# Performance work log

Hardware: AMD Instinct MI355X
Metric: run time of the kernel (lower is better)

Reference implementation:

```python
import jax, jax.numpy as jnp
import numpy as np

B, T, E, H, N = 256, 8, 768, 768, 20000


def setup_inputs() -> dict:
    key = jax.random.key(0)
    ks = jax.random.split(key, 10)
    s = lambda k, shape, sc=1.0: jax.random.normal(k, shape, dtype=jnp.float32) * sc
    return {
        "current_sample_encodings": s(ks[0], (B, E)),
        "example_encodings": s(ks[1], (B, T, E)),
        "all_example_encodings": s(ks[2], (N, E)),
        "policy_example_indices": jax.random.randint(ks[3], (B, T), 0, N, dtype=jnp.int32),
        "W_init": s(ks[4], (E, H), E ** -0.5),
        "b_init": jnp.zeros((H,), jnp.float32),
        "Wx": s(ks[5], (E, 3 * H), E ** -0.5),
        "Wh": s(ks[6], (H, 3 * H), H ** -0.5),
        "bx": jnp.zeros((3 * H,), jnp.float32),
        "bh": jnp.zeros((3 * H,), jnp.float32),
        "bilinear": s(ks[7], (H, E), H ** -0.5),
        "vfe_w": s(ks[8], (H,), H ** -0.5),
        "vfe_b": jnp.zeros((), jnp.float32),
    }


def reference(current_sample_encodings, example_encodings, all_example_encodings,
              policy_example_indices, W_init, b_init, Wx, Wh, bx, bh,
              bilinear, vfe_w, vfe_b):
    Bb, Tt, Ee = example_encodings.shape

    # --- get_latent_states: GRU over example encodings, h0 from current sample ---
    h0 = jnp.tanh(current_sample_encodings @ W_init + b_init)  # [B,H]

    def gru_step(h, x):
        gx = x @ Wx + bx                      # [B,3H]
        gh = h @ Wh + bh                      # [B,3H]
        xr, xz, xn = jnp.split(gx, 3, axis=-1)
        hr, hz, hn = jnp.split(gh, 3, axis=-1)
        r = jax.nn.sigmoid(xr + hr)
        z = jax.nn.sigmoid(xz + hz)
        n = jnp.tanh(xn + r * hn)
        h_new = (1.0 - z) * n + z * h
        return h_new, h_new

    xs = jnp.swapaxes(example_encodings[:, :-1], 0, 1)   # [T-1,B,E]
    _, hs = jax.lax.scan(gru_step, h0, xs)               # [T-1,B,H]
    latent = jnp.concatenate([h0[None], hs], axis=0)     # [T,B,H]

    # --- bilinear query vectors and scoring against the full corpus ---
    query = jnp.einsum('tbh,he->tbe', latent, bilinear)          # [T,B,E]
    acts = jnp.einsum('tbe,ne->tbn', query, all_example_encodings)  # [T,B,N]

    # --- fused scatter masking: -inf at indices of previously chosen examples ---
    neg_inf = jnp.float32(-jnp.inf)

    def mask_step(used, inp):
        a_t, idx_t = inp                                  # [B,N], [B]
        out = jnp.where(used, neg_inf, a_t)
        used = used.at[jnp.arange(Bb), idx_t].set(True)
        return used, out

    used0 = jnp.zeros((Bb, acts.shape[-1]), dtype=bool)
    idxs = jnp.swapaxes(policy_example_indices, 0, 1)     # [T,B]
    _, masked = jax.lax.scan(mask_step, used0, (acts, idxs))  # [T,B,N]

    activations = jnp.swapaxes(masked, 0, 1).reshape(Bb * Tt, -1)  # [B*T,N]

    latent_bt = jnp.swapaxes(latent, 0, 1)                # [B,T,H]
    value_estimates = (latent_bt @ vfe_w + vfe_b).reshape(-1)  # [B*T]
    return activations, value_estimates
```

## Files before the change

### kernel.cpp

```cpp
#include <hip/hip_runtime.h>
#include <math.h>
#include <float.h>

constexpr int Bb = 256, Tt = 8, Ee = 768, Hh = 768, Nn = 20000;
constexpr int H3 = 3 * Hh;

__device__ inline float mask_val() { return __uint_as_float(0xFF7F0000u); }

typedef __attribute__((ext_vector_type(8))) short bf16x8;
typedef __attribute__((ext_vector_type(4))) float f32x4;

__device__ inline unsigned short bf16rne(float x) {
    unsigned u = __float_as_uint(x);
    return (unsigned short)((u + 0x7FFFu + ((u >> 16) & 1)) >> 16);
}
__device__ inline unsigned pk2(float a, float b) {
    return (unsigned)bf16rne(a) | ((unsigned)bf16rne(b) << 16);
}
__device__ inline float sigm(float x) { return 1.f / (1.f + expf(-x)); }

__device__ inline void glds16(const void* g, void* l) {
    __builtin_amdgcn_global_load_lds(
        (const __attribute__((address_space(1))) void*)g,
        (__attribute__((address_space(3))) void*)l, 16, 0, 0);
}

__global__ __launch_bounds__(256) void cvt_all(const float* __restrict__ a, unsigned* __restrict__ oa, int na8,
                                               const float* __restrict__ b, unsigned* __restrict__ ob, int nb8,
                                               const float* __restrict__ c, unsigned* __restrict__ oc, int nc8)
{
    int i = blockIdx.x * 256 + threadIdx.x;
    const float* src; unsigned* dst;
    if (i < na8)            { src = a; dst = oa; }
    else if (i < na8 + nb8) { i -= na8; src = b; dst = ob; }
    else                    { i -= na8 + nb8; if (i >= nc8) return; src = c; dst = oc; }
    const float4* p = (const float4*)(src + (size_t)i * 8);
    float4 x = p[0], y = p[1];
    uint4 v;
    v.x = pk2(x.x, x.y); v.y = pk2(x.z, x.w);
    v.z = pk2(y.x, y.y); v.w = pk2(y.z, y.w);
    *(uint4*)(dst + (size_t)i * 4) = v;
}

__global__ __launch_bounds__(256) void trans_cvt(const float* __restrict__ in, int R, int C,
                                                 unsigned short* __restrict__ out)
{
    __shared__ float tile[32][33];
    int c0 = blockIdx.x * 32, r0 = blockIdx.y * 32;
    int t = threadIdx.x;
    int row = t >> 3, c4 = (t & 7) * 4;
    float4 v = *(const float4*)(in + (size_t)(r0 + row) * C + c0 + c4);
    tile[row][c4+0] = v.x; tile[row][c4+1] = v.y;
    tile[row][c4+2] = v.z; tile[row][c4+3] = v.w;
    __syncthreads();
    int crow = t >> 3, r4 = (t & 7) * 4;
    ushort4 o;
    o.x = bf16rne(tile[r4+0][crow]);
    o.y = bf16rne(tile[r4+1][crow]);
    o.z = bf16rne(tile[r4+2][crow]);
    o.w = bf16rne(tile[r4+3][crow]);
    *(ushort4*)(out + (size_t)(c0 + crow) * R + r0 + r4) = o;
}

__global__ __launch_bounds__(256) void trans_wh(const float* __restrict__ in,
                                                unsigned short* __restrict__ out)
{
    __shared__ float tile[32][33];
    int c0 = blockIdx.x * 32, r0 = blockIdx.y * 32;
    int t = threadIdx.x;
    int row = t >> 3, c4 = (t & 7) * 4;
    float4 v = *(const float4*)(in + (size_t)(r0 + row) * H3 + c0 + c4);
    tile[row][c4+0] = v.x; tile[row][c4+1] = v.y;
    tile[row][c4+2] = v.z; tile[row][c4+3] = v.w;
    __syncthreads();
    int crow = t >> 3, r4 = (t & 7) * 4;
    int cc = c0 + crow;
    int g = cc / Hh, ch = cc - g * Hh;
    int rho = (ch >> 6) * 192 + g * 64 + (ch & 63);
    ushort4 o;
    o.x = bf16rne(tile[r4+0][crow]);
    o.y = bf16rne(tile[r4+1][crow]);
    o.z = bf16rne(tile[r4+2][crow]);
    o.w = bf16rne(tile[r4+3][crow]);
    *(ushort4*)(out + (size_t)rho * Hh + r0 + r4) = o;
}

__global__ __launch_bounds__(256) void gemm_big64(const unsigned short* __restrict__ A,
                                                  const unsigned short* __restrict__ B,
                                                  float* __restrict__ C)
{
    constexpr int BUF = 32768;
    __shared__ char lds[2 * BUF];
    const int t = threadIdx.x;
    const int l = t & 63, w = t >> 6;
    const int wm = (w >> 1) * 64, wn = (w & 1) * 64;

    int id = (blockIdx.x & 7) * 314 + (blockIdx.x >> 3);
    const int bm = (id & 15) * 128;
    const int bn = (id >> 4) * 128;

    const int srow = t >> 3, sslot = t & 7;
    const char* gA[4]; const char* gB[4];
    #pragma unroll
    for (int p = 0; p < 4; ++p) {
        int rp = p * 32 + srow;
        int oct = sslot ^ ((rp >> 1) & 7);
        gA[p] = (const char*)A + (size_t)(bm + rp) * (Ee * 2) + oct * 16;
        int gn = bn + rp; if (gn > Nn - 1) gn = Nn - 1;
        gB[p] = (const char*)B + (size_t)gn * (Ee * 2) + oct * 16;
    }
    const int dbase = t * 16;

    int rAo[4][2], rBo[4][2];
    #pragma unroll
    for (int i = 0; i < 4; ++i) {
        int Ra = wm + i * 16 + (l & 15);
        int Rb = wn + i * 16 + (l & 15);
        #pragma unroll
        for (int ko = 0; ko < 2; ++ko) {
            rAo[i][ko] = Ra * 128 + ((((l >> 4) + 4 * ko) ^ ((Ra >> 1) & 7)) * 16);
            rBo[i][ko] = 16384 + Rb * 128 + ((((l >> 4) + 4 * ko) ^ ((Rb >> 1) & 7)) * 16);
        }
    }

    f32x4 acc[4][4];
    #pragma unroll
    for (int i = 0; i < 4; ++i)
        #pragma unroll
        for (int j = 0; j < 4; ++j)
            acc[i][j] = (f32x4){0.f, 0.f, 0.f, 0.f};

    #pragma unroll
    for (int p = 0; p < 4; ++p) {
        glds16(gA[p], lds + p * 4096 + dbase);
        glds16(gB[p], lds + 16384 + p * 4096 + dbase);
    }
    __syncthreads();

    int cur = 0;
    for (int kt = 0; kt < 12; ++kt) {
        if (kt + 1 < 12) {
            int kb = (kt + 1) * 128;
            char* nb = lds + (cur ^ 1) * BUF;
            #pragma unroll
            for (int p = 0; p < 4; ++p) {
                glds16(gA[p] + kb, nb + p * 4096 + dbase);
                glds16(gB[p] + kb, nb + 16384 + p * 4096 + dbase);
            }
        }
        const char* base = lds + cur * BUF;
        bf16x8 af[4][2], bf[4][2];
        #pragma unroll
        for (int i = 0; i < 4; ++i)
            #pragma unroll
            for (int ko = 0; ko < 2; ++ko) {
                af[i][ko] = *(const bf16x8*)(base + rAo[i][ko]);
                bf[i][ko] = *(const bf16x8*)(base + rBo[i][ko]);
            }
        #pragma unroll
        for (int ko = 0; ko < 2; ++ko)
            #pragma unroll
            for (int i = 0; i < 4; ++i)
                #pragma unroll
                for (int j = 0; j < 4; ++j)
                    acc[i][j] = __builtin_amdgcn_mfma_f32_16x16x32_bf16(af[i][ko], bf[j][ko], acc[i][j], 0, 0, 0);
        __syncthreads();
        cur ^= 1;
    }

    #pragma unroll
    for (int i = 0; i < 4; ++i) {
        int gm = bm + wm + i * 16 + (l >> 4) * 4;
        #pragma unroll
        for (int j = 0; j < 4; ++j) {
            int gn = bn + wn + j * 16 + (l & 15);
            if (gn < Nn) {
                #pragma unroll
                for (int q = 0; q < 4; ++q)
                    C[(size_t)(gm + q) * Nn + gn] = acc[i][j][q];
            }
        }
    }
}

template<int TM, bool CLAMP, bool BIAS, int ACT, int OMODE>
__global__ __launch_bounds__(256) void gemm_mfma(const unsigned short* __restrict__ A, int lda,
                                                 const unsigned short* __restrict__ B,
                                                 const float* __restrict__ bias,
                                                 float* __restrict__ C, int ldc,
                                                 unsigned short* __restrict__ Cbf,
                                                 int M, int N, int K, int nsec)
{
    constexpr int AG  = (TM >= 64) ? TM / 64 : 1;
    constexpr int AB  = TM * 64;
    constexpr int BUF = (TM + 128) * 64;
    constexpr int FM  = (TM >= 64) ? 4 : 2;
    constexpr int FN  = (TM == 128) ? 4 : 2;
    __shared__ char lds[2 * BUF];
    const int t = threadIdx.x;

    int by, bx;
    {
        int id = ((blockIdx.x & 7) * (gridDim.x >> 3)) + (blockIdx.x >> 3);
        by = id / nsec; bx = id - by * nsec;
    }
    const int bm = by * TM, bn = bx * 128;

    const int l = t & 63, w = t >> 6;
    const int wm = (TM == 128) ? (w >> 1) * 64 : 0;
    const int wn = (TM == 128) ? (w & 1) * 64 : w * 32;

    const int sr = w * 16 + (l >> 2);
    const int slot = l & 3;

    const char* gA[AG]; int lA[AG];
    #pragma unroll
    for (int p = 0; p < AG; ++p) {
        int r = p * 64 + sr;
        int rr = (TM == 32) ? (r & 31) : r;
        int oct = slot ^ ((rr >> 1) & 3);
        gA[p] = (const char*)A + (size_t)(bm + rr) * lda * 2 + oct * 16;
        lA[p] = p * 4096 + w * 1024;
    }
    const char* gB[2]; int lB[2];
    #pragma unroll
    for (int p = 0; p < 2; ++p) {
        int r = p * 64 + sr;
        int oct = slot ^ ((r >> 1) & 3);
        int gn = bn + r;
        if (CLAMP) gn = (gn > N - 1) ? (N - 1) : gn;
        gB[p] = (const char*)B + (size_t)gn * K * 2 + oct * 16;
        lB[p] = AB + p * 4096 + w * 1024;
    }

    int rAo[FM], rBo[FN];
    #pragma unroll
    for (int i = 0; i < FM; ++i) {
        int Ra = wm + i * 16 + (l & 15);
        rAo[i] = Ra * 64 + (((l >> 4) ^ ((Ra >> 1) & 3)) * 16);
    }
    #pragma unroll
    for (int j = 0; j < FN; ++j) {
        int Rb = wn + j * 16 + (l & 15);
        rBo[j] = AB + Rb * 64 + (((l >> 4) ^ ((Rb >> 1) & 3)) * 16);
    }

    f32x4 acc[FM][FN];
    #pragma unroll
    for (int i = 0; i < FM; ++i)
        #pragma unroll
        for (int j = 0; j < FN; ++j)
            acc[i][j] = (f32x4){0.f, 0.f, 0.f, 0.f};

    if (TM > 32 || w < 2) {
        #pragma unroll
        for (int p = 0; p < AG; ++p) glds16(gA[p], lds + lA[p]);
    }
    #pragma unroll
    for (int p = 0; p < 2;  ++p) glds16(gB[p], lds + lB[p]);
    __syncthreads();

    int cur = 0;
    for (int k0 = 0; k0 < K; k0 += 32) {
        if (k0 + 32 < K) {
            int kb = (k0 + 32) * 2;
            char* nb = lds + (cur ^ 1) * BUF;
            if (TM > 32 || w < 2) {
                #pragma unroll
                for (int p = 0; p < AG; ++p) glds16(gA[p] + kb, nb + lA[p]);
            }
            #pragma unroll
            for (int p = 0; p < 2;  ++p) glds16(gB[p] + kb, nb + lB[p]);
        }
        const char* base = lds + cur * BUF;
        bf16x8 af[FM], bf[FN];
        #pragma unroll
        for (int i = 0; i < FM; ++i) af[i] = *(const bf16x8*)(base + rAo[i]);
        #pragma unroll
        for (int j = 0; j < FN; ++j) bf[j] = *(const bf16x8*)(base + rBo[j]);
        #pragma unroll
        for (int i = 0; i < FM; ++i)
            #pragma unroll
            for (int j = 0; j < FN; ++j)
                acc[i][j] = __builtin_amdgcn_mfma_f32_16x16x32_bf16(af[i], bf[j], acc[i][j], 0, 0, 0);
        __syncthreads();
        cur ^= 1;
    }

    #pragma unroll
    for (int i = 0; i < FM; ++i) {
        int gm = bm + wm + i * 16 + (l >> 4) * 4;
        #pragma unroll
        for (int j = 0; j < FN; ++j) {
            int gn = bn + wn + j * 16 + (l & 15);
            if (!CLAMP || gn < N) {
                #pragma unroll
                for (int q = 0; q < 4; ++q) {
                    float v = acc[i][j][q];
                    if (BIAS) v += bias[gn];
                    if (ACT == 1) v = tanhf(v);
                    if (OMODE & 1) C[(size_t)(gm + q) * ldc + gn] = v;
                    if (OMODE & 2) Cbf[(size_t)(gm + q) * ldc + gn] = bf16rne(v);
                }
            }
        }
    }
}

__global__ __launch_bounds__(256) void gru_fused(const unsigned short* __restrict__ latbf_t,
                                                 const unsigned short* __restrict__ WhG,
                                                 const float* __restrict__ gx_t,
                                                 const float* __restrict__ bh,
                                                 const float* __restrict__ latent_t,
                                                 float* __restrict__ latent_t1,
                                                 unsigned short* __restrict__ latbf_t1)
{
    constexpr int LDA = Tt * Hh;
    constexpr int LDG = Tt * H3;
    constexpr int ABY = 4096;
    constexpr int BUF = ABY + 24576;
    __shared__ char lds[2 * BUF];
    const int t = threadIdx.x;
    const int mb = blockIdx.x & 7, cb = blockIdx.x >> 3;
    const int bm = mb * 32;

    const int l = t & 63, w = t >> 6;
    const int srow = t >> 3;
    const int sslot = t & 7;

    const char* gA = (const char*)latbf_t + (size_t)(bm + srow) * (LDA * 2)
                   + ((sslot ^ ((srow >> 1) & 7)) * 16);
    const int dA = w * 1024;

    const char* gB[6]; int dB[6];
    #pragma unroll
    for (int p = 0; p < 6; ++p) {
        int rp = p * 32 + srow;
        gB[p] = (const char*)WhG + (size_t)(cb * 192 + rp) * (Hh * 2)
              + ((sslot ^ ((rp >> 1) & 7)) * 16);
        dB[p] = ABY + p * 4096 + w * 1024;
    }

    int rAo[2][2], rBo[3][2];
    #pragma unroll
    for (int i = 0; i < 2; ++i) {
        int Ra = i * 16 + (l & 15);
        #pragma unroll
        for (int ko = 0; ko < 2; ++ko)
            rAo[i][ko] = Ra * 128 + ((((l >> 4) + 4 * ko) ^ ((Ra >> 1) & 7)) * 16);
    }
    #pragma unroll
    for (int g = 0; g < 3; ++g) {
        int Rb = g * 64 + w * 16 + (l & 15);
        #pragma unroll
        for (int ko = 0; ko < 2; ++ko)
            rBo[g][ko] = ABY + Rb * 128 + ((((l >> 4) + 4 * ko) ^ ((Rb >> 1) & 7)) * 16);
    }

    f32x4 acc[2][3];
    #pragma unroll
    for (int i = 0; i < 2; ++i)
        #pragma unroll
        for (int g = 0; g < 3; ++g)
            acc[i][g] = (f32x4){0.f, 0.f, 0.f, 0.f};

    glds16(gA, lds + dA);
    #pragma unroll
    for (int p = 0; p < 6; ++p) glds16(gB[p], lds + dB[p]);
    __syncthreads();

    int cur = 0;
    for (int kt = 0; kt < 12; ++kt) {
        if (kt + 1 < 12) {
            int kb = (kt + 1) * 128;
            char* nb = lds + (cur ^ 1) * BUF;
            glds16(gA + kb, nb + dA);
            #pragma unroll
            for (int p = 0; p < 6; ++p) glds16(gB[p] + kb, nb + dB[p]);
        }
        const char* base = lds + cur * BUF;
        bf16x8 af[2][2], bfr[3][2];
        #pragma unroll
        for (int i = 0; i < 2; ++i)
            #pragma unroll
            for (int ko = 0; ko < 2; ++ko) af[i][ko] = *(const bf16x8*)(base + rAo[i][ko]);
        #pragma unroll
        for (int g = 0; g < 3; ++g)
            #pragma unroll
            for (int ko = 0; ko < 2; ++ko) bfr[g][ko] = *(const bf16x8*)(base + rBo[g][ko]);
        #pragma unroll
        for (int ko = 0; ko < 2; ++ko)
            #pragma unroll
            for (int i = 0; i < 2; ++i)
                #pragma unroll
                for (int g = 0; g < 3; ++g)
                    acc[i][g] = __builtin_amdgcn_mfma_f32_16x16x32_bf16(af[i][ko], bfr[g][ko], acc[i][g], 0, 0, 0);
        __syncthreads();
        cur ^= 1;
    }

    const int colj = cb * 64 + w * 16 + (l & 15);
    const float bhr = bh[colj], bhz = bh[Hh + colj], bhn = bh[2 * Hh + colj];
    #pragma unroll
    for (int i = 0; i < 2; ++i) {
        int row0 = bm + i * 16 + (l >> 4) * 4;
        #pragma unroll
        for (int q = 0; q < 4; ++q) {
            int b = row0 + q;
            const float* gxr = gx_t + (size_t)b * LDG;
            float xr = gxr[colj], xz = gxr[Hh + colj], xn = gxr[2 * Hh + colj];
            float r = sigm(xr + acc[i][0][q] + bhr);
            float z = sigm(xz + acc[i][1][q] + bhz);
            float n = tanhf(xn + r * (acc[i][2][q] + bhn));
            float hprev = latent_t[(size_t)b * LDA + colj];
            float hnew = (1.f - z) * n + z * hprev;
            latent_t1[(size_t)b * LDA + colj] = hnew;
            latbf_t1[(size_t)b * LDA + colj] = bf16rne(hnew);
        }
    }
}

__global__ void mask_kernel(const int* __restrict__ idx, float* __restrict__ out)
{
    int b = threadIdx.x;
    if (b >= Bb) return;
    float mv = mask_val();
    for (int ts = 0; ts < Tt - 1; ++ts) {
        int id = idx[b * Tt + ts];
        for (int t = ts + 1; t < Tt; ++t)
            out[(size_t)(b * Tt + t) * Nn + id] = mv;
    }
}

__global__ void value_kernel(const float* __restrict__ latent,
                             const float* __restrict__ w,
                             const float* __restrict__ b0,
                             float* __restrict__ out)
{
    int row = blockIdx.x;
    int lane = threadIdx.x;
    const float* lr = latent + (size_t)row * Hh;
    float s = 0.f;
    for (int j = lane; j < Hh; j += 64) s += lr[j] * w[j];
    #pragma unroll
    for (int m = 32; m; m >>= 1) s += __shfl_xor(s, m, 64);
    if (lane == 0) out[row] = s + b0[0];
}

extern "C" void kernel_launch(void* const* d_in, const int* in_sizes, int n_in,
                              void* d_out, int out_size, void* d_ws, size_t ws_size,
                              hipStream_t stream)
{
    const float* cur  = (const float*)d_in[0];
    const float* ex   = (const float*)d_in[1];
    const float* alle = (const float*)d_in[2];
    const int*   pidx = (const int*)  d_in[3];
    const float* Wi   = (const float*)d_in[4];
    const float* bi   = (const float*)d_in[5];
    const float* Wx   = (const float*)d_in[6];
    const float* Wh   = (const float*)d_in[7];
    const float* bx   = (const float*)d_in[8];
    const float* bh   = (const float*)d_in[9];
    const float* bil  = (const float*)d_in[10];
    const float* vw   = (const float*)d_in[11];
    const float* vb   = (const float*)d_in[12];
    float* out = (float*)d_out;

    float* ws     = (float*)d_ws;
    float* latent = ws;
    float* gx_all = latent + (size_t)Bb*Tt*Hh;
    float* ghb    = gx_all + (size_t)Bb*Tt*H3;
    float* query  = ghb    + (size_t)Bb*H3;
    unsigned short* alle_bf  = (unsigned short*)(query + (size_t)Bb*Tt*Ee);
    unsigned short* query_bf = alle_bf  + (size_t)Nn*Ee;
    unsigned short* ex_bf    = query_bf + (size_t)Bb*Tt*Ee;
    unsigned short* cur_bf   = ex_bf    + (size_t)Bb*Tt*Ee;
    unsigned short* lat_bf   = cur_bf   + (size_t)Bb*Ee;
    unsigned short* WiT_bf   = lat_bf   + (size_t)Bb*Tt*Hh;
    unsigned short* WxT_bf   = WiT_bf   + (size_t)Hh*Ee;
    unsigned short* WhG_bf   = WxT_bf   + (size_t)H3*Ee;
    unsigned short* bilT_bf  = WhG_bf   + (size_t)H3*Hh;

    dim3 blk(256);

    {
        int na8 = Nn*Ee/8, nb8 = Bb*Tt*Ee/8, nc8 = Bb*Ee/8;
        cvt_all<<<dim3((na8+nb8+nc8+255)/256), blk, 0, stream>>>(
            alle, (unsigned*)alle_bf, na8, ex, (unsigned*)ex_bf, nb8,
            cur, (unsigned*)cur_bf, nc8);
    }
    trans_cvt<<<dim3(Hh/32, Ee/32), blk, 0, stream>>>(Wi,  Ee, Hh, WiT_bf);
    trans_cvt<<<dim3(H3/32, Ee/32), blk, 0, stream>>>(Wx,  Ee, H3, WxT_bf);
    trans_wh <<<dim3(H3/32, Hh/32), blk, 0, stream>>>(Wh,  WhG_bf);
    trans_cvt<<<dim3(Ee/32, Hh/32), blk, 0, stream>>>(bil, Hh, Ee, bilT_bf);

    gemm_mfma<32,false,true,1,3><<<dim3((Bb/32)*(Hh/128)), blk, 0, stream>>>(
        cur_bf, Ee, WiT_bf, bi, latent, Tt*Hh, lat_bf, Bb, Hh, Ee, Hh/128);

    gemm_mfma<128,false,true,0,1><<<dim3((Bb*Tt/128)*(H3/128)), blk, 0, stream>>>(
        ex_bf, Ee, WxT_bf, bx, gx_all, H3, nullptr, Bb*Tt, H3, Ee, H3/128);

    for (int t = 0; t < Tt - 1; ++t) {
        gru_fused<<<dim3(96), blk, 0, stream>>>(
            lat_bf + (size_t)t*Hh, WhG_bf, gx_all + (size_t)t*H3, bh,
            latent + (size_t)t*Hh, latent + (size_t)(t+1)*Hh, lat_bf + (size_t)(t+1)*Hh);
    }

    gemm_mfma<128,false,false,0,2><<<dim3((Bb*Tt/128)*(Ee/128)), blk, 0, stream>>>(
        lat_bf, Hh, bilT_bf, nullptr, query, Ee, query_bf, Bb*Tt, Ee, Hh, Ee/128);

    gemm_big64<<<dim3(157*16), blk, 0, stream>>>(query_bf, alle_bf, out);

    mask_kernel<<<dim3(1), blk, 0, stream>>>(pidx, out);
    value_kernel<<<dim3(Bb*Tt), dim3(64), 0, stream>>>(latent, vw, vb,
                                                       out + (size_t)Bb*Tt*Nn);
}
```

Before: 253.0 us.

## Triple-buffer big scoring GEMM with K=32 stages and single barrier per step

Replaces the double-buffered 128-wide K-tile pipeline of the large corpus-scoring GEMM with a three-stage ring of 64-wide K tiles. It prefetches two tiles ahead, waits on vmcnt explicitly and uses one barrier per iteration instead of two syncs. The goal is to overlap global-to-LDS loads with MFMA work better and to halve the LDS footprint, which may allow more blocks per CU. The cost is twice as many iterations and barriers, and it relies on the vmcnt counting being right for correctness.

```diff
diff --git a/kernel.cpp b/kernel.cpp
--- a/kernel.cpp
+++ b/kernel.cpp
@@ -24,6 +24,8 @@
         (const __attribute__((address_space(1))) void*)g,
         (__attribute__((address_space(3))) void*)l, 16, 0, 0);
 }
+
+#define SCHED __builtin_amdgcn_sched_barrier(0)
 
 __global__ __launch_bounds__(256) void cvt_all(const float* __restrict__ a, unsigned* __restrict__ oa, int na8,
                                                const float* __restrict__ b, unsigned* __restrict__ ob, int nb8,
@@ -85,12 +87,13 @@
     *(ushort4*)(out + (size_t)rho * Hh + r0 + r4) = o;
 }
 
-__global__ __launch_bounds__(256) void gemm_big64(const unsigned short* __restrict__ A,
-                                                  const unsigned short* __restrict__ B,
-                                                  float* __restrict__ C)
-{
-    constexpr int BUF = 32768;
-    __shared__ char lds[2 * BUF];
+__global__ __launch_bounds__(256) void gemm_bigp(const unsigned short* __restrict__ A,
+                                                 const unsigned short* __restrict__ B,
+                                                 float* __restrict__ C)
+{
+    constexpr int NT  = 24;
+    constexpr int BUF = 16384;
+    __shared__ char lds[3 * BUF];
     const int t = threadIdx.x;
     const int l = t & 63, w = t >> 6;
     const int wm = (w >> 1) * 64, wn = (w & 1) * 64;
@@ -99,28 +102,28 @@
     const int bm = (id & 15) * 128;
     const int bn = (id >> 4) * 128;
 
-    const int srow = t >> 3, sslot = t & 7;
-    const char* gA[4]; const char* gB[4];
-    #pragma unroll
-    for (int p = 0; p < 4; ++p) {
-        int rp = p * 32 + srow;
-        int oct = sslot ^ ((rp >> 1) & 7);
-        gA[p] = (const char*)A + (size_t)(bm + rp) * (Ee * 2) + oct * 16;
-        int gn = bn + rp; if (gn > Nn - 1) gn = Nn - 1;
+    const int sr = w * 16 + (l >> 2);
+    const int slot = l & 3;
+    const char* gA[2]; const char* gB[2];
+    int dA[2], dB[2];
+    #pragma unroll
+    for (int p = 0; p < 2; ++p) {
+        int r = p * 64 + sr;
+        int oct = slot ^ ((r >> 1) & 3);
+        gA[p] = (const char*)A + (size_t)(bm + r) * (Ee * 2) + oct * 16;
+        dA[p] = p * 4096 + w * 1024;
+        int gn = bn + r; if (gn > Nn - 1) gn = Nn - 1;
         gB[p] = (const char*)B + (size_t)gn * (Ee * 2) + oct * 16;
-    }
-    const int dbase = t * 16;
-
-    int rAo[4][2], rBo[4][2];
+        dB[p] = 8192 + p * 4096 + w * 1024;
+    }
+
+    int rAo[4], rBo[4];
     #pragma unroll
     for (int i = 0; i < 4; ++i) {
         int Ra = wm + i * 16 + (l & 15);
         int Rb = wn + i * 16 + (l & 15);
-        #pragma unroll
-        for (int ko = 0; ko < 2; ++ko) {
-            rAo[i][ko] = Ra * 128 + ((((l >> 4) + 4 * ko) ^ ((Ra >> 1) & 7)) * 16);
-            rBo[i][ko] = 16384 + Rb * 128 + ((((l >> 4) + 4 * ko) ^ ((Rb >> 1) & 7)) * 16);
-        }
+        rAo[i] = Ra * 64 + (((l >> 4) ^ ((Ra >> 1) & 3)) * 16);
+        rBo[i] = 8192 + Rb * 64 + (((l >> 4) ^ ((Rb >> 1) & 3)) * 16);
     }
 
     f32x4 acc[4][4];
@@ -131,41 +134,36 @@
             acc[i][j] = (f32x4){0.f, 0.f, 0.f, 0.f};
 
     #pragma unroll
-    for (int p = 0; p < 4; ++p) {
-        glds16(gA[p], lds + p * 4096 + dbase);
-        glds16(gB[p], lds + 16384 + p * 4096 + dbase);
-    }
-    __syncthreads();
-
-    int cur = 0;
-    for (int kt = 0; kt < 12; ++kt) {
-        if (kt + 1 < 12) {
-            int kb = (kt + 1) * 128;
-            char* nb = lds + (cur ^ 1) * BUF;
-            #pragma unroll
-            for (int p = 0; p < 4; ++p) {
-                glds16(gA[p] + kb, nb + p * 4096 + dbase);
-                glds16(gB[p] + kb, nb + 16384 + p * 4096 + dbase);
-            }
+    for (int p = 0; p < 2; ++p) { glds16(gA[p], lds + dA[p]); glds16(gB[p], lds + dB[p]); }
+    #pragma unroll
+    for (int p = 0; p < 2; ++p) { glds16(gA[p] + 64, lds + BUF + dA[p]);
+                                  glds16(gB[p] + 64, lds + BUF + dB[p]); }
+
+    #pragma unroll 3
+    for (int kt = 0; kt < NT; ++kt) {
+        if (kt < NT - 1) asm volatile("s_waitcnt vmcnt(4)" ::: "memory");
+        else             asm volatile("s_waitcnt vmcnt(0)" ::: "memory");
+        SCHED;
+        __builtin_amdgcn_s_barrier();
+        SCHED;
+        const char* base = lds + (kt % 3) * BUF;
+        bf16x8 af[4], bf[4];
+        #pragma unroll
+        for (int i = 0; i < 4; ++i) af[i] = *(const bf16x8*)(base + rAo[i]);
+        #pragma unroll
+        for (int j = 0; j < 4; ++j) bf[j] = *(const bf16x8*)(base + rBo[j]);
+        if (kt + 2 < NT) {
+            int kb = (kt + 2) * 64;
+            char* nb = lds + ((kt + 2) % 3) * BUF;
+            #pragma unroll
+            for (int p = 0; p < 2; ++p) { glds16(gA[p] + kb, nb + dA[p]);
+                                          glds16(gB[p] + kb, nb + dB[p]); }
         }
-        const char* base = lds + cur * BUF;
-        bf16x8 af[4][2], bf[4][2];
         #pragma unroll
         for (int i = 0; i < 4; ++i)
             #pragma unroll
-            for (int ko = 0; ko < 2; ++ko) {
-                af[i][ko] = *(const bf16x8*)(base + rAo[i][ko]);
-                bf[i][ko] = *(const bf16x8*)(base + rBo[i][ko]);
-            }
-        #pragma unroll
-        for (int ko = 0; ko < 2; ++ko)
-            #pragma unroll
-            for (int i = 0; i < 4; ++i)
-                #pragma unroll
-                for (int j = 0; j < 4; ++j)
-                    acc[i][j] = __builtin_amdgcn_mfma_f32_16x16x32_bf16(af[i][ko], bf[j][ko], acc[i][j], 0, 0, 0);
-        __syncthreads();
-        cur ^= 1;
+            for (int j = 0; j < 4; ++j)
+                acc[i][j] = __builtin_amdgcn_mfma_f32_16x16x32_bf16(af[i], bf[j], acc[i][j], 0, 0, 0);
     }
 
     #pragma unroll
@@ -509,7 +507,7 @@
     gemm_mfma<128,false,false,0,2><<<dim3((Bb*Tt/128)*(Ee/128)), blk, 0, stream>>>(
         lat_bf, Hh, bilT_bf, nullptr, query, Ee, query_bf, Bb*Tt, Ee, Hh, Ee/128);
 
-    gemm_big64<<<dim3(157*16), blk, 0, stream>>>(query_bf, alle_bf, out);
+    gemm_bigp<<<dim3(157*16), blk, 0, stream>>>(query_bf, alle_bf, out);
 
     mask_kernel<<<dim3(1), blk, 0, stream>>>(pidx, out);
     value_kernel<<<dim3(Bb*Tt), dim3(64), 0, stream>>>(latent, vw, vb,
```

Measured after the change: 268.4 us. 6.1% more time.

## Persist GRU steps in one kernel with grid barriers and merge small launches

Applied to the files above, without the earlier changes.

Replaces the seven per-timestep GRU launches with one persistent kernel. Each of its 96 blocks loops over time and syncs with the other 12 column blocks of its batch slice through a global atomic counter. The four weight transpose kernels are merged into one launch, and the mask and value-head kernels into another. The aim is to cut launch overhead and inter-kernel gaps on the serial GRU chain. The spin barrier assumes all 96 blocks are co-resident and needs an extra memset of the counters.

```diff
diff --git a/kernel.cpp b/kernel.cpp
--- a/kernel.cpp
+++ b/kernel.cpp
@@ -42,11 +42,24 @@
     *(uint4*)(dst + (size_t)i * 4) = v;
 }
 
-__global__ __launch_bounds__(256) void trans_cvt(const float* __restrict__ in, int R, int C,
-                                                 unsigned short* __restrict__ out)
+__global__ __launch_bounds__(256) void trans4(const float* __restrict__ Wi,
+                                              const float* __restrict__ Wx,
+                                              const float* __restrict__ Wh,
+                                              const float* __restrict__ bil,
+                                              unsigned short* __restrict__ WiT,
+                                              unsigned short* __restrict__ WxT,
+                                              unsigned short* __restrict__ WhG,
+                                              unsigned short* __restrict__ bilT)
 {
     __shared__ float tile[32][33];
-    int c0 = blockIdx.x * 32, r0 = blockIdx.y * 32;
+    int b = blockIdx.x;
+    const float* in; unsigned short* outp; int C; bool wh = false; int bx, by;
+    if (b < 576)       { in = Wi;  outp = WiT;  C = Ee; bx = b % 24; by = b / 24; }
+    else if (b < 2304) { b -= 576;  in = Wx;  outp = WxT;  C = H3; bx = b % 72; by = b / 72; }
+    else if (b < 4032) { b -= 2304; in = Wh;  outp = WhG;  C = H3; bx = b % 72; by = b / 72; wh = true; }
+    else               { b -= 4032; in = bil; outp = bilT; C = Hh; bx = b % 24; by = b / 24; }
+
+    int c0 = bx * 32, r0 = by * 32;
     int t = threadIdx.x;
     int row = t >> 3, c4 = (t & 7) * 4;
     float4 v = *(const float4*)(in + (size_t)(r0 + row) * C + c0 + c4);
@@ -54,35 +67,20 @@
     tile[row][c4+2] = v.z; tile[row][c4+3] = v.w;
     __syncthreads();
     int crow = t >> 3, r4 = (t & 7) * 4;
+    int cc = c0 + crow;
+    int orow;
+    if (wh) {
+        int g = cc / Hh, ch = cc - g * Hh;
+        orow = (ch >> 6) * 192 + g * 64 + (ch & 63);
+    } else {
+        orow = cc;
+    }
     ushort4 o;
     o.x = bf16rne(tile[r4+0][crow]);
     o.y = bf16rne(tile[r4+1][crow]);
     o.z = bf16rne(tile[r4+2][crow]);
     o.w = bf16rne(tile[r4+3][crow]);
-    *(ushort4*)(out + (size_t)(c0 + crow) * R + r0 + r4) = o;
-}
-
-__global__ __launch_bounds__(256) void trans_wh(const float* __restrict__ in,
-                                                unsigned short* __restrict__ out)
-{
-    __shared__ float tile[32][33];
-    int c0 = blockIdx.x * 32, r0 = blockIdx.y * 32;
-    int t = threadIdx.x;
-    int row = t >> 3, c4 = (t & 7) * 4;
-    float4 v = *(const float4*)(in + (size_t)(r0 + row) * H3 + c0 + c4);
-    tile[row][c4+0] = v.x; tile[row][c4+1] = v.y;
-    tile[row][c4+2] = v.z; tile[row][c4+3] = v.w;
-    __syncthreads();
-    int crow = t >> 3, r4 = (t & 7) * 4;
-    int cc = c0 + crow;
-    int g = cc / Hh, ch = cc - g * Hh;
-    int rho = (ch >> 6) * 192 + g * 64 + (ch & 63);
-    ushort4 o;
-    o.x = bf16rne(tile[r4+0][crow]);
-    o.y = bf16rne(tile[r4+1][crow]);
-    o.z = bf16rne(tile[r4+2][crow]);
-    o.w = bf16rne(tile[r4+3][crow]);
-    *(ushort4*)(out + (size_t)rho * Hh + r0 + r4) = o;
+    *(ushort4*)(outp + (size_t)orow * 768 + r0 + r4) = o;
 }
 
 __global__ __launch_bounds__(256) void gemm_big64(const unsigned short* __restrict__ A,
@@ -307,29 +305,27 @@
     }
 }
 
-__global__ __launch_bounds__(256) void gru_fused(const unsigned short* __restrict__ latbf_t,
+__global__ __launch_bounds__(256) void gru_chain(const unsigned short* __restrict__ lat_bf,
                                                  const unsigned short* __restrict__ WhG,
-                                                 const float* __restrict__ gx_t,
+                                                 const float* __restrict__ gx_all,
                                                  const float* __restrict__ bh,
-                                                 const float* __restrict__ latent_t,
-                                                 float* __restrict__ latent_t1,
-                                                 unsigned short* __restrict__ latbf_t1)
-{
-    constexpr int LDA = Tt * Hh;
-    constexpr int LDG = Tt * H3;
+                                                 float* __restrict__ latent,
+                                                 unsigned short* __restrict__ latbf_w,
+                                                 int* __restrict__ bar)
+{
     constexpr int ABY = 4096;
     constexpr int BUF = ABY + 24576;
     __shared__ char lds[2 * BUF];
-    const int t = threadIdx.x;
+    const int t0 = threadIdx.x;
     const int mb = blockIdx.x & 7, cb = blockIdx.x >> 3;
     const int bm = mb * 32;
 
-    const int l = t & 63, w = t >> 6;
-    const int srow = t >> 3;
-    const int sslot = t & 7;
-
-    const char* gA = (const char*)latbf_t + (size_t)(bm + srow) * (LDA * 2)
-                   + ((sslot ^ ((srow >> 1) & 7)) * 16);
+    const int l = t0 & 63, w = t0 >> 6;
+    const int srow = t0 >> 3;
+    const int sslot = t0 & 7;
+
+    const char* gA0 = (const char*)lat_bf + (size_t)(bm + srow) * (Tt * Hh * 2)
+                    + ((sslot ^ ((srow >> 1) & 7)) * 16);
     const int dA = w * 1024;
 
     const char* gB[6]; int dB[6];
@@ -357,94 +353,111 @@
             rBo[g][ko] = ABY + Rb * 128 + ((((l >> 4) + 4 * ko) ^ ((Rb >> 1) & 7)) * 16);
     }
 
-    f32x4 acc[2][3];
-    #pragma unroll
-    for (int i = 0; i < 2; ++i)
-        #pragma unroll
-        for (int g = 0; g < 3; ++g)
-            acc[i][g] = (f32x4){0.f, 0.f, 0.f, 0.f};
-
-    glds16(gA, lds + dA);
-    #pragma unroll
-    for (int p = 0; p < 6; ++p) glds16(gB[p], lds + dB[p]);
-    __syncthreads();
-
-    int cur = 0;
-    for (int kt = 0; kt < 12; ++kt) {
-        if (kt + 1 < 12) {
-            int kb = (kt + 1) * 128;
-            char* nb = lds + (cur ^ 1) * BUF;
-            glds16(gA + kb, nb + dA);
-            #pragma unroll
-            for (int p = 0; p < 6; ++p) glds16(gB[p] + kb, nb + dB[p]);
-        }
-        const char* base = lds + cur * BUF;
-        bf16x8 af[2][2], bfr[3][2];
-        #pragma unroll
-        for (int i = 0; i < 2; ++i)
-            #pragma unroll
-            for (int ko = 0; ko < 2; ++ko) af[i][ko] = *(const bf16x8*)(base + rAo[i][ko]);
-        #pragma unroll
-        for (int g = 0; g < 3; ++g)
-            #pragma unroll
-            for (int ko = 0; ko < 2; ++ko) bfr[g][ko] = *(const bf16x8*)(base + rBo[g][ko]);
-        #pragma unroll
-        for (int ko = 0; ko < 2; ++ko)
-            #pragma unroll
-            for (int i = 0; i < 2; ++i)
-                #pragma unroll
-                for (int g = 0; g < 3; ++g)
-                    acc[i][g] = __builtin_amdgcn_mfma_f32_16x16x32_bf16(af[i][ko], bfr[g][ko], acc[i][g], 0, 0, 0);
-        __syncthreads();
-        cur ^= 1;
-    }
-
     const int colj = cb * 64 + w * 16 + (l & 15);
     const float bhr = bh[colj], bhz = bh[Hh + colj], bhn = bh[2 * Hh + colj];
-    #pragma unroll
-    for (int i = 0; i < 2; ++i) {
-        int row0 = bm + i * 16 + (l >> 4) * 4;
-        #pragma unroll
-        for (int q = 0; q < 4; ++q) {
-            int b = row0 + q;
-            const float* gxr = gx_t + (size_t)b * LDG;
-            float xr = gxr[colj], xz = gxr[Hh + colj], xn = gxr[2 * Hh + colj];
-            float r = sigm(xr + acc[i][0][q] + bhr);
-            float z = sigm(xz + acc[i][1][q] + bhz);
-            float n = tanhf(xn + r * (acc[i][2][q] + bhn));
-            float hprev = latent_t[(size_t)b * LDA + colj];
-            float hnew = (1.f - z) * n + z * hprev;
-            latent_t1[(size_t)b * LDA + colj] = hnew;
-            latbf_t1[(size_t)b * LDA + colj] = bf16rne(hnew);
-        }
-    }
-}
-
-__global__ void mask_kernel(const int* __restrict__ idx, float* __restrict__ out)
-{
-    int b = threadIdx.x;
-    if (b >= Bb) return;
-    float mv = mask_val();
-    for (int ts = 0; ts < Tt - 1; ++ts) {
-        int id = idx[b * Tt + ts];
-        for (int t = ts + 1; t < Tt; ++t)
-            out[(size_t)(b * Tt + t) * Nn + id] = mv;
-    }
-}
-
-__global__ void value_kernel(const float* __restrict__ latent,
-                             const float* __restrict__ w,
-                             const float* __restrict__ b0,
-                             float* __restrict__ out)
-{
-    int row = blockIdx.x;
-    int lane = threadIdx.x;
-    const float* lr = latent + (size_t)row * Hh;
-    float s = 0.f;
-    for (int j = lane; j < Hh; j += 64) s += lr[j] * w[j];
-    #pragma unroll
-    for (int m = 32; m; m >>= 1) s += __shfl_xor(s, m, 64);
-    if (lane == 0) out[row] = s + b0[0];
+
+    for (int t = 0; t < Tt - 1; ++t) {
+        const char* gA = gA0 + (size_t)t * (Hh * 2);
+
+        f32x4 acc[2][3];
+        #pragma unroll
+        for (int i = 0; i < 2; ++i)
+            #pragma unroll
+            for (int g = 0; g < 3; ++g)
+                acc[i][g] = (f32x4){0.f, 0.f, 0.f, 0.f};
+
+        glds16(gA, lds + dA);
+        #pragma unroll
+        for (int p = 0; p < 6; ++p) glds16(gB[p], lds + dB[p]);
+        __syncthreads();
+
+        int cur = 0;
+        for (int kt = 0; kt < 12; ++kt) {
+            if (kt + 1 < 12) {
+                int kb = (kt + 1) * 128;
+                char* nb = lds + (cur ^ 1) * BUF;
+                glds16(gA + kb, nb + dA);
+                #pragma unroll
+                for (int p = 0; p < 6; ++p) glds16(gB[p] + kb, nb + dB[p]);
+            }
+            const char* base = lds + cur * BUF;
+            bf16x8 af[2][2], bfr[3][2];
+            #pragma unroll
+            for (int i = 0; i < 2; ++i)
+                #pragma unroll
+                for (int ko = 0; ko < 2; ++ko) af[i][ko] = *(const bf16x8*)(base + rAo[i][ko]);
+            #pragma unroll
+            for (int g = 0; g < 3; ++g)
+                #pragma unroll
+                for (int ko = 0; ko < 2; ++ko) bfr[g][ko] = *(const bf16x8*)(base + rBo[g][ko]);
+            #pragma unroll
+            for (int ko = 0; ko < 2; ++ko)
+                #pragma unroll
+                for (int i = 0; i < 2; ++i)
+                    #pragma unroll
+                    for (int g = 0; g < 3; ++g)
+                        acc[i][g] = __builtin_amdgcn_mfma_f32_16x16x32_bf16(af[i][ko], bfr[g][ko], acc[i][g], 0, 0, 0);
+            __syncthreads();
+            cur ^= 1;
+        }
+
+        #pragma unroll
+        for (int i = 0; i < 2; ++i) {
+            int row0 = bm + i * 16 + (l >> 4) * 4;
+            #pragma unroll
+            for (int q = 0; q < 4; ++q) {
+                int b = row0 + q;
+                const float* gxr = gx_all + (size_t)(b * Tt + t) * H3;
+                float xr = gxr[colj], xz = gxr[Hh + colj], xn = gxr[2 * Hh + colj];
+                float r = sigm(xr + acc[i][0][q] + bhr);
+                float z = sigm(xz + acc[i][1][q] + bhz);
+                float n = tanhf(xn + r * (acc[i][2][q] + bhn));
+                float hprev = latent[(size_t)(b * Tt + t) * Hh + colj];
+                float hnew = (1.f - z) * n + z * hprev;
+                latent[(size_t)(b * Tt + t + 1) * Hh + colj] = hnew;
+                latbf_w[(size_t)(b * Tt + t + 1) * Hh + colj] = bf16rne(hnew);
+            }
+        }
+
+        if (t < Tt - 2) {
+            __syncthreads();
+            if (t0 == 0) {
+                __threadfence();
+                __hip_atomic_fetch_add(bar + mb, 1, __ATOMIC_RELEASE, __HIP_MEMORY_SCOPE_AGENT);
+                int target = 12 * (t + 1);
+                while (__hip_atomic_load(bar + mb, __ATOMIC_ACQUIRE, __HIP_MEMORY_SCOPE_AGENT) < target) {}
+                __threadfence();
+            }
+            __syncthreads();
+        }
+    }
+}
+
+__global__ __launch_bounds__(256) void maskval(const int* __restrict__ idx,
+                                               const float* __restrict__ latent,
+                                               const float* __restrict__ vw,
+                                               const float* __restrict__ vb,
+                                               float* __restrict__ out)
+{
+    if (blockIdx.x < 512) {
+        int row = blockIdx.x * 4 + (threadIdx.x >> 6);
+        int lane = threadIdx.x & 63;
+        const float* lr = latent + (size_t)row * Hh;
+        float s = 0.f;
+        for (int j = lane; j < Hh; j += 64) s += lr[j] * vw[j];
+        #pragma unroll
+        for (int m = 32; m; m >>= 1) s += __shfl_xor(s, m, 64);
+        if (lane == 0) out[(size_t)Bb * Tt * Nn + row] = s + vb[0];
+    } else {
+        int b = threadIdx.x;
+        if (b >= Bb) return;
+        float mv = mask_val();
+        for (int ts = 0; ts < Tt - 1; ++ts) {
+            int id = idx[b * Tt + ts];
+            for (int t = ts + 1; t < Tt; ++t)
+                out[(size_t)(b * Tt + t) * Nn + id] = mv;
+        }
+    }
 }
 
 extern "C" void kernel_launch(void* const* d_in, const int* in_sizes, int n_in,
@@ -480,8 +493,11 @@
     unsigned short* WxT_bf   = WiT_bf   + (size_t)Hh*Ee;
     unsigned short* WhG_bf   = WxT_bf   + (size_t)H3*Ee;
     unsigned short* bilT_bf  = WhG_bf   + (size_t)H3*Hh;
+    int* bar = (int*)(bilT_bf + (size_t)Ee*Hh);
 
     dim3 blk(256);
+
+    hipMemsetAsync(bar, 0, 8 * sizeof(int), stream);
 
     {
         int na8 = Nn*Ee/8, nb8 = Bb*Tt*Ee/8, nc8 = Bb*Ee/8;
@@ -489,10 +505,7 @@
             alle, (unsigned*)alle_bf, na8, ex, (unsigned*)ex_bf, nb8,
             cur, (unsigned*)cur_bf, nc8);
     }
-    trans_cvt<<<dim3(Hh/32, Ee/32), blk, 0, stream>>>(Wi,  Ee, Hh, WiT_bf);
-    trans_cvt<<<dim3(H3/32, Ee/32), blk, 0, stream>>>(Wx,  Ee, H3, WxT_bf);
-    trans_wh <<<dim3(H3/32, Hh/32), blk, 0, stream>>>(Wh,  WhG_bf);
-    trans_cvt<<<dim3(Ee/32, Hh/32), blk, 0, stream>>>(bil, Hh, Ee, bilT_bf);
+    trans4<<<dim3(4608), blk, 0, stream>>>(Wi, Wx, Wh, bil, WiT_bf, WxT_bf, WhG_bf, bilT_bf);
 
     gemm_mfma<32,false,true,1,3><<<dim3((Bb/32)*(Hh/128)), blk, 0, stream>>>(
         cur_bf, Ee, WiT_bf, bi, latent, Tt*Hh, lat_bf, Bb, Hh, Ee, Hh/128);
@@ -500,18 +513,13 @@
     gemm_mfma<128,false,true,0,1><<<dim3((Bb*Tt/128)*(H3/128)), blk, 0, stream>>>(
         ex_bf, Ee, WxT_bf, bx, gx_all, H3, nullptr, Bb*Tt, H3, Ee, H3/128);
 
-    for (int t = 0; t < Tt - 1; ++t) {
-        gru_fused<<<dim3(96), blk, 0, stream>>>(
-            lat_bf + (size_t)t*Hh, WhG_bf, gx_all + (size_t)t*H3, bh,
-            latent + (size_t)t*Hh, latent + (size_t)(t+1)*Hh, lat_bf + (size_t)(t+1)*Hh);
-    }
+    gru_chain<<<dim3(96), blk, 0, stream>>>(lat_bf, WhG_bf, gx_all, bh,
+                                            latent, lat_bf, bar);
 
     gemm_mfma<128,false,false,0,2><<<dim3((Bb*Tt/128)*(Ee/128)), blk, 0, stream>>>(
         lat_bf, Hh, bilT_bf, nullptr, query, Ee, query_bf, Bb*Tt, Ee, Hh, Ee/128);
 
     gemm_big64<<<dim3(157*16), blk, 0, stream>>>(query_bf, alle_bf, out);
 
-    mask_kernel<<<dim3(1), blk, 0, stream>>>(pidx, out);
-    value_kernel<<<dim3(Bb*Tt), dim3(64), 0, stream>>>(latent, vw, vb,
-                                                       out + (size_t)Bb*Tt*Nn);
-}
+    maskval<<<dim3(513), blk, 0, stream>>>(pidx, latent, vw, vb, out);
+}
```

Result: slower. 282.0 us (+11.5%).
